# Kernel optimization log

Measured on AMD Instinct MI355X. Metric: run time of the kernel, lower is better.

## Reference

```python
import jax, jax.numpy as jnp
import numpy as np

N = 8192
NHID = 256

def setup_inputs() -> dict:
    key = jax.random.key(0)
    ks = jax.random.split(key, 9)
    s = 1.0 / np.sqrt(NHID)  # torch Linear default init scale
    return {
        "x1": jax.random.normal(ks[0], (N, NHID), jnp.float32),
        "x2": jax.random.normal(ks[1], (N, NHID), jnp.float32),
        "x3": jax.random.normal(ks[2], (N, NHID), jnp.float32),
        "Wq": jax.random.uniform(ks[3], (NHID, NHID), jnp.float32, -s, s),
        "bq": jax.random.uniform(ks[4], (NHID,), jnp.float32, -s, s),
        "Wk": jax.random.uniform(ks[5], (NHID, NHID), jnp.float32, -s, s),
        "bk": jax.random.uniform(ks[6], (NHID,), jnp.float32, -s, s),
        "Wv": jax.random.uniform(ks[7], (NHID, NHID), jnp.float32, -s, s),
        "bv": jax.random.uniform(ks[8], (NHID,), jnp.float32, -s, s),
    }

def reference(x1, x2, x3, Wq, bq, Wk, bk, Wv, bv):
    # torch.nn.Linear: y = x @ W.T + b
    q = x1 @ Wq.T + bq                      # [N, nhid]
    k = x2 @ Wk.T + bk                      # [N, nhid]
    v = x3 @ Wv.T + bv                      # [N, nhid]
    scores = q @ k.T                        # [N, N], NOTE: unscaled (no 1/sqrt(d))
    attn = jax.nn.softmax(scores, axis=1)   # softmax over keys (dim=1)
    return attn @ v                         # [N, nhid]
```

## Files before the change

### kernel.cpp

```cpp
#include <hip/hip_runtime.h>
#include <stdint.h>

typedef unsigned short u16;
typedef __attribute__((ext_vector_type(8))) short short8;
typedef __attribute__((ext_vector_type(4))) float f32x4;

#define LOG2E 1.4426950408889634f
#define NT 8192
#define DH 256

#define QH     0
#define KH     2097152
#define VTB    4194304
#define OPARTB 6291456
#define XH0 6291456
#define XL0 8388608
#define XH1 10485760
#define XL1 12582912
#define XH2 14680064
#define XL2 16777216
#define WQH 18874368
#define WQL 18939904
#define WKH 19005440
#define WKL 19070976
#define WVH 19136512
#define WVL 19202048
#define MPART_F 11534336
#define LPART_F 11599872

__device__ __forceinline__ u16 f2bf(float f) {
  union { float f; uint32_t u; } c; c.f = f;
  uint32_t u = c.u;
  return (u16)((u + 0x7fffu + ((u >> 16) & 1)) >> 16);
}
__device__ __forceinline__ u16 f2bf_hu(float f) {
  union { float f; uint32_t u; } c; c.f = f;
  return (u16)((c.u + 0x8000u) >> 16);
}
__device__ __forceinline__ float bf2f(u16 h) {
  union { uint32_t u; float f; } c; c.u = ((uint32_t)h) << 16;
  return c.f;
}

__device__ __forceinline__ int swz32(int u, int row) {
  return (u & 24) | ((u & 7) ^ (row & 7));
}

__device__ __forceinline__ f32x4 mfma16(short8 a, short8 b, f32x4 c) {
  return __builtin_amdgcn_mfma_f32_16x16x32_bf16(a, b, c, 0, 0, 0);
}

__device__ __forceinline__ void gl_lds16(const u16* g, u16* l) {
  __builtin_amdgcn_global_load_lds(
      (const __attribute__((address_space(1))) uint32_t*)g,
      (__attribute__((address_space(3))) uint32_t*)l, 16, 0, 0);
}

__global__ __launch_bounds__(256) void k_convert(
    const float* __restrict__ x1, const float* __restrict__ x2, const float* __restrict__ x3,
    const float* __restrict__ wq, const float* __restrict__ wk, const float* __restrict__ wv,
    u16* __restrict__ wsu) {
  int b = blockIdx.x;
  const float* src; u16 *dh, *dl; int bl;
  if (b < 1024)      { src = x1; dh = wsu + XH0; dl = wsu + XL0; bl = b; }
  else if (b < 2048) { src = x2; dh = wsu + XH1; dl = wsu + XL1; bl = b - 1024; }
  else if (b < 3072) { src = x3; dh = wsu + XH2; dl = wsu + XL2; bl = b - 2048; }
  else if (b < 3104) { src = wq; dh = wsu + WQH; dl = wsu + WQL; bl = b - 3072; }
  else if (b < 3136) { src = wk; dh = wsu + WKH; dl = wsu + WKL; bl = b - 3104; }
  else               { src = wv; dh = wsu + WVH; dl = wsu + WVL; bl = b - 3136; }
  int i = (bl * 256 + threadIdx.x) * 8;
  f32x4 a = *(const f32x4*)(src + i);
  f32x4 c = *(const f32x4*)(src + i + 4);
  short8 rh, rl;
  float v[8] = {a[0], a[1], a[2], a[3], c[0], c[1], c[2], c[3]};
#pragma unroll
  for (int j = 0; j < 8; j++) {
    u16 h = f2bf(v[j]);
    rh[j] = (short)h;
    rl[j] = (short)f2bf(v[j] - bf2f(h));
  }
  *(short8*)(dh + i) = rh;
  *(short8*)(dl + i) = rl;
}

__global__ __launch_bounds__(256) void k_qkv(
    u16* __restrict__ wsu,
    const float* __restrict__ bq, const float* __restrict__ bk, const float* __restrict__ bv) {
  __shared__ u16 sAh[64 * 256];
  __shared__ u16 sAl[64 * 256];
  int bx = blockIdx.x;
  int mid = bx >> 10;
  int t = bx & 1023;
  const u16 *Ah, *Al, *Bh, *Bl; u16 *Ohi; const float* bias;
  int rb, cb, ldO, biasRow;
  if (mid == 0) {
    Ah = wsu + XH0; Al = wsu + XL0; Bh = wsu + WQH; Bl = wsu + WQL;
    Ohi = wsu + QH; bias = bq; biasRow = 0; ldO = 256;
    rb = t >> 3; cb = t & 7;
  } else if (mid == 1) {
    Ah = wsu + XH1; Al = wsu + XL1; Bh = wsu + WKH; Bl = wsu + WKL;
    Ohi = wsu + KH; bias = bk; biasRow = 0; ldO = 256;
    rb = t >> 3; cb = t & 7;
  } else {
    Ah = wsu + WVH; Al = wsu + WVL; Bh = wsu + XH2; Bl = wsu + XL2;
    Ohi = wsu + VTB; bias = bv; biasRow = 1; ldO = 8192;
    rb = t >> 8; cb = t & 255;
  }

  int tid = threadIdx.x;
#pragma unroll
  for (int i = 0; i < 8; i++) {
    int L = i * 256 + tid;
    int row = L >> 5, u = L & 31;
    short8 vh = *(const short8*)(Ah + (rb * 64 + row) * 256 + u * 8);
    short8 vl = *(const short8*)(Al + (rb * 64 + row) * 256 + u * 8);
    *(short8*)(&sAh[row * 256 + swz32(u, row) * 8]) = vh;
    *(short8*)(&sAl[row * 256 + swz32(u, row) * 8]) = vl;
  }

  int lane = tid & 63, wave = tid >> 6;
  int n = lane & 15, quad = lane >> 4;
  int wm = wave >> 1, wn = wave & 1;
  int col0 = cb * 32 + wn * 16;
  const u16* pBh = Bh + (size_t)(col0 + n) * 256 + quad * 8;
  const u16* pBl = Bl + (size_t)(col0 + n) * 256 + quad * 8;

  __syncthreads();

  f32x4 acc0 = {0.f,0.f,0.f,0.f}, acc1 = {0.f,0.f,0.f,0.f};
#pragma unroll
  for (int kk = 0; kk < 8; kk++) {
    int ra = wm * 32 + n;
    int sa0 = ra * 256 + swz32(kk * 4 + quad, ra) * 8;
    int sa1 = (ra + 16) * 256 + swz32(kk * 4 + quad, ra + 16) * 8;
    short8 a0h = *(const short8*)(&sAh[sa0]);
    short8 a1h = *(const short8*)(&sAh[sa1]);
    short8 a0l = *(const short8*)(&sAl[sa0]);
    short8 a1l = *(const short8*)(&sAl[sa1]);
    short8 bh  = *(const short8*)(pBh + kk * 32);
    short8 bl  = *(const short8*)(pBl + kk * 32);
    acc0 = mfma16(a0h, bh, acc0);
    acc1 = mfma16(a1h, bh, acc1);
    acc0 = mfma16(a0h, bl, acc0);
    acc1 = mfma16(a1h, bl, acc1);
    acc0 = mfma16(a0l, bh, acc0);
    acc1 = mfma16(a1l, bh, acc1);
  }
  int colg = col0 + n;
  float bcol = biasRow ? 0.0f : bias[colg];
#pragma unroll
  for (int mt = 0; mt < 2; mt++) {
    f32x4 acc = mt ? acc1 : acc0;
#pragma unroll
    for (int r = 0; r < 4; r++) {
      int rowg = rb * 64 + wm * 32 + mt * 16 + quad * 4 + r;
      float bb = biasRow ? bias[rowg] : bcol;
      Ohi[(size_t)rowg * ldO + colg] = f2bf(acc[r] + bb);
    }
  }
}

__global__ __launch_bounds__(256, 2) void k_flash(
    const u16* __restrict__ wsu, u16* __restrict__ opart, float* __restrict__ wsf) {
  __shared__ u16 sK[2][32 * 256];
  __shared__ u16 sV[2][256 * 32];
  __shared__ u16 sP[4 * 32 * 40];

  int qb = blockIdx.x >> 3, sp = blockIdx.x & 7;
  int tid = threadIdx.x, lane = tid & 63, wave = tid >> 6;
  int n = lane & 15, quad = lane >> 4;
  const u16* Qp = wsu + QH;
  const u16* Kp = wsu + KH;
  const u16* Vp = wsu + VTB;

  short8 qf[2][8];
  int rowQ0 = qb * 128 + wave * 32 + n;
#pragma unroll
  for (int mt = 0; mt < 2; mt++)
#pragma unroll
    for (int kk = 0; kk < 8; kk++)
      qf[mt][kk] = *(const short8*)(Qp + (size_t)(rowQ0 + mt * 16) * 256 + kk * 32 + quad * 8);

  int krow_base = wave * 2 + (lane >> 5);
  int kgu = (lane & 24) | ((lane & 7) ^ (krow_base & 7));
  int vd_base = wave * 16 + (lane >> 2);
  int vgu = (lane & 3) ^ ((lane >> 3) & 3);

  int key00 = sp * 1024;

#pragma unroll
  for (int i = 0; i < 4; i++) {
    gl_lds16(Kp + (size_t)(key00 + i * 8 + krow_base) * 256 + kgu * 8,
             &sK[0][i * 2048 + wave * 512]);
    gl_lds16(Vp + (size_t)(i * 64 + vd_base) * 8192 + key00 + vgu * 8,
             &sV[0][i * 2048 + wave * 512]);
  }

  f32x4 o[2][16];
#pragma unroll
  for (int mt = 0; mt < 2; mt++)
#pragma unroll
    for (int nt = 0; nt < 16; nt++) { o[mt][nt][0]=0.f; o[mt][nt][1]=0.f; o[mt][nt][2]=0.f; o[mt][nt][3]=0.f; }
  float negm0L[8], lcur[8];
#pragma unroll
  for (int j = 0; j < 8; j++) { negm0L[j] = 0.f; lcur[j] = 0.f; }

  for (int it = 0; it < 32; it++) {
    __syncthreads();
    int cur = it & 1;
    if (it + 1 < 32) {
      int k1 = key00 + (it + 1) * 32;
#pragma unroll
      for (int i = 0; i < 4; i++) {
        gl_lds16(Kp + (size_t)(k1 + i * 8 + krow_base) * 256 + kgu * 8,
                 &sK[cur ^ 1][i * 2048 + wave * 512]);
        gl_lds16(Vp + (size_t)(i * 64 + vd_base) * 8192 + k1 + vgu * 8,
                 &sV[cur ^ 1][i * 2048 + wave * 512]);
      }
    }

    f32x4 s00={0.f,0.f,0.f,0.f}, s01={0.f,0.f,0.f,0.f};
    f32x4 s10={0.f,0.f,0.f,0.f}, s11={0.f,0.f,0.f,0.f};
#pragma unroll
    for (int kk = 0; kk < 8; kk++) {
      int su = swz32(kk * 4 + quad, n) * 8;
      short8 b0 = *(const short8*)(&sK[cur][n * 256 + su]);
      short8 b1 = *(const short8*)(&sK[cur][(n + 16) * 256 + su]);
      s00 = mfma16(qf[0][kk], b0, s00);
      s01 = mfma16(qf[0][kk], b1, s01);
      s10 = mfma16(qf[1][kk], b0, s10);
      s11 = mfma16(qf[1][kk], b1, s11);
    }

    if (it == 0) {
#pragma unroll
      for (int mt = 0; mt < 2; mt++)
#pragma unroll
        for (int r = 0; r < 4; r++) {
          float v = mt ? fmaxf(s10[r], s11[r]) : fmaxf(s00[r], s01[r]);
          v = fmaxf(v, __shfl_xor(v, 1));
          v = fmaxf(v, __shfl_xor(v, 2));
          v = fmaxf(v, __shfl_xor(v, 4));
          v = fmaxf(v, __shfl_xor(v, 8));
          negm0L[mt * 4 + r] = -v * LOG2E;
        }
    }

    u16* myP = &sP[wave * 1280];
#pragma unroll
    for (int mt = 0; mt < 2; mt++)
#pragma unroll
      for (int r = 0; r < 4; r++) {
        int j = mt * 4 + r;
        float sv0 = mt ? s10[r] : s00[r];
        float sv1 = mt ? s11[r] : s01[r];
        float x0 = fminf(fmaf(sv0, LOG2E, negm0L[j]), 110.f);
        float x1 = fminf(fmaf(sv1, LOG2E, negm0L[j]), 110.f);
        float p0 = exp2f(x0);
        float p1 = exp2f(x1);
        lcur[j] += p0 + p1;
        int row = mt * 16 + quad * 4 + r;
        myP[row * 40 + n] = f2bf_hu(p0);
        myP[row * 40 + 16 + n] = f2bf_hu(p1);
      }

    u16* myP2 = &sP[wave * 1280];
    short8 pa0 = *(const short8*)(&myP2[n * 40 + quad * 8]);
    short8 pa1 = *(const short8*)(&myP2[(16 + n) * 40 + quad * 8]);
#pragma unroll
    for (int nt = 0; nt < 16; nt++) {
      int d = nt * 16 + n;
      short8 vb = *(const short8*)(&sV[cur][d * 32 + (quad ^ ((n >> 1) & 3)) * 8]);
      o[0][nt] = mfma16(pa0, vb, o[0][nt]);
      o[1][nt] = mfma16(pa1, vb, o[1][nt]);
    }
  }

#pragma unroll
  for (int j = 0; j < 8; j++) {
    float v = lcur[j];
    v += __shfl_xor(v, 1); v += __shfl_xor(v, 2);
    v += __shfl_xor(v, 4); v += __shfl_xor(v, 8);
    lcur[j] = v;
  }

  u16* op = opart + (size_t)sp * (NT * DH);
  int rowb = qb * 128 + wave * 32;
#pragma unroll
  for (int mt = 0; mt < 2; mt++)
#pragma unroll
    for (int nt = 0; nt < 16; nt++)
#pragma unroll
      for (int r = 0; r < 4; r++) {
        int row = rowb + mt * 16 + quad * 4 + r;
        op[(size_t)row * 256 + nt * 16 + n] = f2bf(o[mt][nt][r]);
      }
  if (n == 0) {
#pragma unroll
    for (int j = 0; j < 8; j++) {
      int row = rowb + (j >> 2) * 16 + quad * 4 + (j & 3);
      wsf[MPART_F + sp * NT + row] = negm0L[j] * -0.6931471805599453f;
      wsf[LPART_F + sp * NT + row] = lcur[j];
    }
  }
}

__global__ __launch_bounds__(256) void k_combine(
    const u16* __restrict__ opart, const float* __restrict__ wsf, float* __restrict__ out) {
  int gid = blockIdx.x * 256 + threadIdx.x;
  int row = gid >> 6, cg = gid & 63;
  float m[8], l[8];
#pragma unroll
  for (int s = 0; s < 8; s++) {
    m[s] = wsf[MPART_F + s * NT + row];
    l[s] = wsf[LPART_F + s * NT + row];
  }
  float ms = m[0];
#pragma unroll
  for (int s = 1; s < 8; s++) ms = fmaxf(ms, m[s]);
  float denom = 0.f;
  float acc[4] = {0.f, 0.f, 0.f, 0.f};
#pragma unroll
  for (int s = 0; s < 8; s++) {
    float w = exp2f((m[s] - ms) * LOG2E);
    denom += w * l[s];
    const u16* pp = opart + ((size_t)s * NT + row) * 256 + cg * 4;
    uint2 v = *(const uint2*)pp;
    acc[0] += w * bf2f((u16)(v.x & 0xffff));
    acc[1] += w * bf2f((u16)(v.x >> 16));
    acc[2] += w * bf2f((u16)(v.y & 0xffff));
    acc[3] += w * bf2f((u16)(v.y >> 16));
  }
  float inv = 1.0f / denom;
  f32x4 r = {acc[0] * inv, acc[1] * inv, acc[2] * inv, acc[3] * inv};
  *(f32x4*)(out + (size_t)row * 256 + cg * 4) = r;
}

extern "C" void kernel_launch(void* const* d_in, const int* in_sizes, int n_in,
                              void* d_out, int out_size, void* d_ws, size_t ws_size,
                              hipStream_t stream) {
  const float* x1 = (const float*)d_in[0];
  const float* x2 = (const float*)d_in[1];
  const float* x3 = (const float*)d_in[2];
  const float* Wq = (const float*)d_in[3];
  const float* bq = (const float*)d_in[4];
  const float* Wk = (const float*)d_in[5];
  const float* bk = (const float*)d_in[6];
  const float* Wv = (const float*)d_in[7];
  const float* bv = (const float*)d_in[8];
  u16* wsu = (u16*)d_ws;
  float* wsf = (float*)d_ws;
  float* out = (float*)d_out;

  k_convert<<<dim3(3168), dim3(256), 0, stream>>>(x1, x2, x3, Wq, Wk, Wv, wsu);
  k_qkv<<<dim3(3072), dim3(256), 0, stream>>>(wsu, bq, bk, bv);
  k_flash<<<dim3(512), dim3(256), 0, stream>>>(wsu, wsu + OPARTB, wsf);
  k_combine<<<dim3(2048), dim3(256), 0, stream>>>(wsu + OPARTB, wsf, out);
}
```

Measured before the change: 230.0 us.

## Retile QKV projection so each block stages 32 A rows and loops over 256 columns

The QKV projection kernel now stages a 32-row A tile in shared memory once and loops over four 64-column chunks, covering 256 output columns per block instead of a 64x32 tile. The grid shrinks from 3072 to 768 blocks. This cuts the redundant global-to-LDS reloads of the A operand, which were repeated for every column block. The cost is fewer blocks, a serial loop per block, and less parallelism available to hide B-operand global load latency.

```diff
diff --git a/kernel.cpp b/kernel.cpp
--- a/kernel.cpp
+++ b/kernel.cpp
@@ -86,76 +86,74 @@
 __global__ __launch_bounds__(256) void k_qkv(
     u16* __restrict__ wsu,
     const float* __restrict__ bq, const float* __restrict__ bk, const float* __restrict__ bv) {
-  __shared__ u16 sAh[64 * 256];
-  __shared__ u16 sAl[64 * 256];
+  __shared__ u16 sAh[32 * 256];
+  __shared__ u16 sAl[32 * 256];
   int bx = blockIdx.x;
-  int mid = bx >> 10;
-  int t = bx & 1023;
-  const u16 *Ah, *Al, *Bh, *Bl; u16 *Ohi; const float* bias;
-  int rb, cb, ldO, biasRow;
+  int mid = bx >> 8;
+  int t = bx & 255;
+  const u16 *Ah, *Al, *Bh, *Bl; u16 *O; const float* bias;
+  int rowA0, col0, ldO, biasRow;
   if (mid == 0) {
     Ah = wsu + XH0; Al = wsu + XL0; Bh = wsu + WQH; Bl = wsu + WQL;
-    Ohi = wsu + QH; bias = bq; biasRow = 0; ldO = 256;
-    rb = t >> 3; cb = t & 7;
+    O = wsu + QH; bias = bq; biasRow = 0; ldO = 256;
+    rowA0 = t * 32; col0 = 0;
   } else if (mid == 1) {
     Ah = wsu + XH1; Al = wsu + XL1; Bh = wsu + WKH; Bl = wsu + WKL;
-    Ohi = wsu + KH; bias = bk; biasRow = 0; ldO = 256;
-    rb = t >> 3; cb = t & 7;
+    O = wsu + KH; bias = bk; biasRow = 0; ldO = 256;
+    rowA0 = t * 32; col0 = 0;
   } else {
     Ah = wsu + WVH; Al = wsu + WVL; Bh = wsu + XH2; Bl = wsu + XL2;
-    Ohi = wsu + VTB; bias = bv; biasRow = 1; ldO = 8192;
-    rb = t >> 8; cb = t & 255;
+    O = wsu + VTB; bias = bv; biasRow = 1; ldO = 8192;
+    rowA0 = (t & 7) * 32; col0 = (t >> 3) * 256;
   }
 
   int tid = threadIdx.x;
 #pragma unroll
-  for (int i = 0; i < 8; i++) {
+  for (int i = 0; i < 4; i++) {
     int L = i * 256 + tid;
     int row = L >> 5, u = L & 31;
-    short8 vh = *(const short8*)(Ah + (rb * 64 + row) * 256 + u * 8);
-    short8 vl = *(const short8*)(Al + (rb * 64 + row) * 256 + u * 8);
+    short8 vh = *(const short8*)(Ah + (size_t)(rowA0 + row) * 256 + u * 8);
+    short8 vl = *(const short8*)(Al + (size_t)(rowA0 + row) * 256 + u * 8);
     *(short8*)(&sAh[row * 256 + swz32(u, row) * 8]) = vh;
     *(short8*)(&sAl[row * 256 + swz32(u, row) * 8]) = vl;
   }
+  __syncthreads();
 
   int lane = tid & 63, wave = tid >> 6;
   int n = lane & 15, quad = lane >> 4;
-  int wm = wave >> 1, wn = wave & 1;
-  int col0 = cb * 32 + wn * 16;
-  const u16* pBh = Bh + (size_t)(col0 + n) * 256 + quad * 8;
-  const u16* pBl = Bl + (size_t)(col0 + n) * 256 + quad * 8;
-
-  __syncthreads();
-
-  f32x4 acc0 = {0.f,0.f,0.f,0.f}, acc1 = {0.f,0.f,0.f,0.f};
-#pragma unroll
-  for (int kk = 0; kk < 8; kk++) {
-    int ra = wm * 32 + n;
-    int sa0 = ra * 256 + swz32(kk * 4 + quad, ra) * 8;
-    int sa1 = (ra + 16) * 256 + swz32(kk * 4 + quad, ra + 16) * 8;
-    short8 a0h = *(const short8*)(&sAh[sa0]);
-    short8 a1h = *(const short8*)(&sAh[sa1]);
-    short8 a0l = *(const short8*)(&sAl[sa0]);
-    short8 a1l = *(const short8*)(&sAl[sa1]);
-    short8 bh  = *(const short8*)(pBh + kk * 32);
-    short8 bl  = *(const short8*)(pBl + kk * 32);
-    acc0 = mfma16(a0h, bh, acc0);
-    acc1 = mfma16(a1h, bh, acc1);
-    acc0 = mfma16(a0h, bl, acc0);
-    acc1 = mfma16(a1h, bl, acc1);
-    acc0 = mfma16(a0l, bh, acc0);
-    acc1 = mfma16(a1l, bh, acc1);
-  }
-  int colg = col0 + n;
-  float bcol = biasRow ? 0.0f : bias[colg];
-#pragma unroll
-  for (int mt = 0; mt < 2; mt++) {
-    f32x4 acc = mt ? acc1 : acc0;
-#pragma unroll
-    for (int r = 0; r < 4; r++) {
-      int rowg = rb * 64 + wm * 32 + mt * 16 + quad * 4 + r;
-      float bb = biasRow ? bias[rowg] : bcol;
-      Ohi[(size_t)rowg * ldO + colg] = f2bf(acc[r] + bb);
+
+#pragma unroll 1
+  for (int itc = 0; itc < 4; itc++) {
+    int colg = col0 + itc * 64 + wave * 16 + n;
+    const u16* pBh = Bh + (size_t)colg * 256 + quad * 8;
+    const u16* pBl = Bl + (size_t)colg * 256 + quad * 8;
+    f32x4 acc0 = {0.f,0.f,0.f,0.f}, acc1 = {0.f,0.f,0.f,0.f};
+#pragma unroll
+    for (int kk = 0; kk < 8; kk++) {
+      int su = swz32(kk * 4 + quad, n) * 8;
+      short8 a0h = *(const short8*)(&sAh[n * 256 + su]);
+      short8 a1h = *(const short8*)(&sAh[(n + 16) * 256 + su]);
+      short8 a0l = *(const short8*)(&sAl[n * 256 + su]);
+      short8 a1l = *(const short8*)(&sAl[(n + 16) * 256 + su]);
+      short8 bh  = *(const short8*)(pBh + kk * 32);
+      short8 bl  = *(const short8*)(pBl + kk * 32);
+      acc0 = mfma16(a0h, bh, acc0);
+      acc1 = mfma16(a1h, bh, acc1);
+      acc0 = mfma16(a0h, bl, acc0);
+      acc1 = mfma16(a1h, bl, acc1);
+      acc0 = mfma16(a0l, bh, acc0);
+      acc1 = mfma16(a1l, bh, acc1);
+    }
+    float bcol = biasRow ? 0.0f : bias[colg];
+#pragma unroll
+    for (int mt = 0; mt < 2; mt++) {
+      f32x4 acc = mt ? acc1 : acc0;
+#pragma unroll
+      for (int r = 0; r < 4; r++) {
+        int rowg = rowA0 + mt * 16 + quad * 4 + r;
+        float bb = biasRow ? bias[rowg] : bcol;
+        O[(size_t)rowg * ldO + colg] = f2bf(acc[r] + bb);
+      }
     }
   }
 }
@@ -353,7 +351,7 @@
   float* out = (float*)d_out;
 
   k_convert<<<dim3(3168), dim3(256), 0, stream>>>(x1, x2, x3, Wq, Wk, Wv, wsu);
-  k_qkv<<<dim3(3072), dim3(256), 0, stream>>>(wsu, bq, bk, bv);
+  k_qkv<<<dim3(768), dim3(256), 0, stream>>>(wsu, bq, bk, bv);
   k_flash<<<dim3(512), dim3(256), 0, stream>>>(wsu, wsu + OPARTB, wsf);
   k_combine<<<dim3(2048), dim3(256), 0, stream>>>(wsu + OPARTB, wsf, out);
 }
```

Result: faster. 223.8 us (-2.7%).
